# Kernel tuning notes

Hardware: AMD Instinct MI355X
Metric: run time of the kernel (lower is better)

Reference implementation:

```python
import jax, jax.numpy as jnp
import numpy as np

BN_EPS = 1e-5


def setup_inputs() -> dict:
    key = jax.random.key(0)
    ks = jax.random.split(key, 10)
    D, N, NDRUG, NTAIL, NREL = 256, 128, 572, 100000, 100
    return {
        "drug_table": jax.random.normal(ks[0], (NDRUG, D), jnp.float32),
        "rela_table": jax.random.normal(ks[1], (NREL, D), jnp.float32),
        "ent_table": jax.random.normal(ks[2], (NTAIL, D), jnp.float32),
        "W1": jax.random.normal(ks[3], (NDRUG, D, D), jnp.float32),
        "b1": jax.random.normal(ks[4], (N, D), jnp.float32),
        "W2": jax.random.normal(ks[5], (NDRUG, D, D), jnp.float32),
        "b2": jax.random.normal(ks[6], (N, D), jnp.float32),
        "lin_w": jax.random.normal(ks[7], (D, 2 * D), jnp.float32) * (1.0 / np.sqrt(2 * D)),
        "lin_b": jnp.zeros((D,), jnp.float32),
        "bn_gamma": jnp.ones((D,), jnp.float32),
        "bn_beta": jnp.zeros((D,), jnp.float32),
        "drug_name": jnp.arange(NDRUG, dtype=jnp.int64) if jax.config.jax_enable_x64 else jnp.arange(NDRUG, dtype=jnp.int32),
        "adj_tail": jax.random.randint(ks[8], (NDRUG, N), 0, NTAIL, jnp.int32),
        "adj_relation": jax.random.randint(ks[9], (NDRUG, N), 0, NREL, jnp.int32),
    }


def reference(drug_table, rela_table, ent_table, W1, b1, W2, b2,
              lin_w, lin_b, bn_gamma, bn_beta,
              drug_name, adj_tail, adj_relation):
    d = drug_table[drug_name]            # (572, D)
    r = rela_table[adj_relation]         # (572, N, D)
    e = ent_table[adj_tail]              # (572, N, D)

    dr = d[:, None, :] * r               # (572, N, D)
    h = jax.nn.relu(jnp.einsum('bnd,bde->bne', dr, W1) + b1)
    h = jnp.einsum('bnd,bde->bne', h, W2) + b2
    score = jax.nn.softmax(jnp.sum(h, axis=-1), axis=1)   # (572, N)
    w_ent = jnp.einsum('bn,bnd->bd', score, e)             # (572, D)

    x = jnp.concatenate([w_ent, d], axis=1)                # (572, 2D)
    y = jax.nn.relu(x @ lin_w.T + lin_b)                   # (572, D)
    # BatchNorm1d in training mode: batch stats, biased variance
    mean = jnp.mean(y, axis=0)
    var = jnp.var(y, axis=0)
    return bn_gamma * (y - mean) * jax.lax.rsqrt(var + BN_EPS) + bn_beta
```

## Files before the change

kernel.cpp:

```cpp
#include <hip/hip_runtime.h>
#include <math.h>

#define DD   256
#define NN   128
#define NB   572
#define NREL 100
#define KS   32
#define NKS  (DD / KS)
#define EH   128
#define RS   80
#define PSS  132
#define LDRUGS 8

typedef _Float16 h8 __attribute__((ext_vector_type(8)));
typedef _Float16 h2 __attribute__((ext_vector_type(2)));
typedef float    f4 __attribute__((ext_vector_type(4)));

__device__ __forceinline__ float4 ld4(const float* p) {
    return *reinterpret_cast<const float4*>(p);
}
__device__ __forceinline__ void split16(float x, _Float16& hi, _Float16& lo) {
    hi = (_Float16)x;
    lo = (_Float16)(x - (float)hi);
}
__device__ __forceinline__ int slotx(int blk2, int row) {
    return ((blk2 ^ (row & 7)) & 7) * 8;
}

__global__ __launch_bounds__(256)
void sum_rows(const float* __restrict__ W2, const float* __restrict__ b2,
              float* __restrict__ w2s, float* __restrict__ b2s)
{
    const int blk  = blockIdx.x;
    const int tid  = threadIdx.x;
    const int lane = tid & 63;
    const int wv   = tid >> 6;

    if (blk < 2 * NB) {
        const int b = blk >> 1, half = blk & 1;
        const float* src = W2 + (size_t)b * DD * DD + (size_t)half * (DD / 2) * DD;
        float* dst = w2s + (size_t)b * DD + half * (DD / 2);
        for (int r = wv; r < DD / 2; r += 4) {
            float4 v = ld4(&src[r * DD + lane * 4]);
            float s = v.x + v.y + v.z + v.w;
            #pragma unroll
            for (int m = 32; m >= 1; m >>= 1) s += __shfl_xor(s, m, 64);
            if (lane == 0) dst[r] = s;
        }
    } else {
        for (int r = wv; r < NN; r += 4) {
            float4 v = ld4(&b2[r * DD + lane * 4]);
            float s = v.x + v.y + v.z + v.w;
            #pragma unroll
            for (int m = 32; m >= 1; m >>= 1) s += __shfl_xor(s, m, 64);
            if (lane == 0) b2s[r] = s;
        }
    }
}

__global__ __launch_bounds__(512, 4)
void gnn_mm(const float* __restrict__ drug_table,
            const float* __restrict__ rela_table,
            const float* __restrict__ W1,
            const float* __restrict__ b1,
            const int*   __restrict__ drug_name,
            const int*   __restrict__ adj_relation,
            const float* __restrict__ w2s_g,
            float* __restrict__ part)
{
    __shared__ __align__(16) _Float16 AB_l[2 * 128 * RS];
    __shared__ float d_l[DD];
    __shared__ float w2s_l[EH];
    __shared__ int   rel_l[NN], urel_l[NN], head_l[NN], next_l[NN];
    __shared__ int   map_l[NREL];
    __shared__ int   U_l, c0_l;

    _Float16* A_l = AB_l;
    _Float16* B_l = AB_l + 128 * RS;
    float*    Pl  = reinterpret_cast<float*>(AB_l);

    const int bid  = blockIdx.x;
    const int b    = bid >> 1, h = bid & 1;
    const int tid  = threadIdx.x;
    const int lane = tid & 63;
    const int wv   = tid >> 6;
    const int rg   = wv >> 2;
    const int cg   = wv & 3;
    const int r16  = lane & 15;
    const int gb   = lane >> 4;

    if (tid < NN) { rel_l[tid] = adj_relation[b * NN + tid]; head_l[tid] = -1; }
    if (tid < NREL) map_l[tid] = -1;
    if (tid < DD)  d_l[tid] = drug_table[(size_t)drug_name[b] * DD + tid];
    if (tid >= DD && tid < DD + EH)
        w2s_l[tid - DD] = w2s_g[(size_t)b * DD + h * EH + (tid - DD)];
    __syncthreads();
    if (tid < NN) map_l[rel_l[tid]] = 1;
    __syncthreads();

    bool mk = false; int rank = 0, tot = 0;
    if (tid < 128) {
        mk = (tid < NREL) && (map_l[tid] != -1);
        unsigned long long bal = __ballot(mk);
        rank = __popcll(bal & ((1ull << (tid & 63)) - 1));
        tot  = __popcll(bal);
    }
    if (tid < 64) {
        if (mk) { map_l[tid] = rank; urel_l[rank] = tid; }
        if (tid == 0) c0_l = tot;
    }
    __syncthreads();
    if (tid >= 64 && tid < 128) {
        const int base = c0_l;
        if (mk) { map_l[tid] = base + rank; urel_l[base + rank] = tid; }
        if (tid == 64) U_l = base + tot;
    }
    __syncthreads();
    if (tid < NN)
        next_l[tid] = atomicExch(&head_l[map_l[rel_l[tid]]], tid);
    __syncthreads();

    const int U   = U_l;
    const int NRT = (U + 31) >> 5;

    const float* W1b = W1 + (size_t)b * DD * DD;

    {
        const int padrows = NRT * 32 - U;
        h8 z = {(_Float16)0.f,(_Float16)0.f,(_Float16)0.f,(_Float16)0.f,
                (_Float16)0.f,(_Float16)0.f,(_Float16)0.f,(_Float16)0.f};
        for (int x = tid; x < padrows * 8; x += 512) {
            int r = U + (x >> 3), c = (x & 7) * 8;
            *(h8*)&A_l[r * RS + c] = z;
        }
    }

    const int kb  = (tid >> 7) & 3;
    const int be  = tid & 127;
    const int sau = tid >> 2;
    const int sab = tid & 3;

    float rbv[8];
    float4 raA, raB;

    #define STAGE_LOAD(kt_) {                                                  \
        const int k0_ = (kt_) * KS + kb * 8;                                   \
        const float* wp = &W1b[(size_t)k0_ * DD + h * EH + be];                \
        _Pragma("unroll")                                                      \
        for (int j = 0; j < 8; ++j) rbv[j] = wp[(size_t)j * DD];               \
        if (sau < U) {                                                         \
            const float* rr = rela_table + (size_t)urel_l[sau] * DD            \
                              + (kt_) * KS + sab * 8;                          \
            raA = ld4(rr); raB = ld4(rr + 4);                                  \
        }                                                                      \
    }

    #define STAGE_WRITE(kt_) {                                                 \
        const int k0_ = (kt_) * KS + kb * 8;                                   \
        h8 hv, lv;                                                             \
        _Pragma("unroll")                                                      \
        for (int j = 0; j < 8; ++j) {                                          \
            _Float16 hh, ll;                                                   \
            split16(rbv[j] * d_l[k0_ + j], hh, ll);                            \
            hv[j] = hh; lv[j] = ll;                                            \
        }                                                                      \
        *(h8*)&B_l[be * RS + slotx(2 * kb,     be)] = hv;                      \
        *(h8*)&B_l[be * RS + slotx(2 * kb + 1, be)] = lv;                      \
        if (sau < U) {                                                         \
            const float vr[8] = {raA.x, raA.y, raA.z, raA.w,                   \
                                 raB.x, raB.y, raB.z, raB.w};                  \
            h8 ahv, alv;                                                       \
            _Pragma("unroll")                                                  \
            for (int j = 0; j < 8; ++j) {                                      \
                _Float16 hh, ll;                                               \
                split16(vr[j], hh, ll);                                        \
                ahv[j] = hh; alv[j] = ll;                                      \
            }                                                                  \
            *(h8*)&A_l[sau * RS + slotx(2 * sab,     sau)] = ahv;              \
            *(h8*)&A_l[sau * RS + slotx(2 * sab + 1, sau)] = alv;              \
        }                                                                      \
    }

    STAGE_LOAD(0);
    STAGE_WRITE(0);
    __syncthreads();

    f4 acc[2][2][2];
    #pragma unroll
    for (int p = 0; p < 2; ++p)
        #pragma unroll
        for (int sr = 0; sr < 2; ++sr)
            #pragma unroll
            for (int sc = 0; sc < 2; ++sc)
                acc[p][sr][sc] = {0.f, 0.f, 0.f, 0.f};

    for (int kt = 0; kt < NKS; ++kt) {
        if (kt + 1 < NKS) STAGE_LOAD(kt + 1);

        h8 bh[2], bl[2];
        #pragma unroll
        for (int sc = 0; sc < 2; ++sc) {
            const int e = cg * 32 + sc * 16 + r16;
            bh[sc] = *(const h8*)&B_l[e * RS + slotx(2 * gb,     e)];
            bl[sc] = *(const h8*)&B_l[e * RS + slotx(2 * gb + 1, e)];
        }
        #pragma unroll
        for (int p = 0; p < 2; ++p) {
            const int rt = rg + 2 * p;
            if (rt < NRT) {
                #pragma unroll
                for (int sr = 0; sr < 2; ++sr) {
                    const int row = rt * 32 + sr * 16 + r16;
                    h8 ah = *(const h8*)&A_l[row * RS + slotx(2 * gb,     row)];
                    h8 al = *(const h8*)&A_l[row * RS + slotx(2 * gb + 1, row)];
                    #pragma unroll
                    for (int sc = 0; sc < 2; ++sc) {
                        acc[p][sr][sc] = __builtin_amdgcn_mfma_f32_16x16x32_f16(ah, bh[sc], acc[p][sr][sc], 0, 0, 0);
                        acc[p][sr][sc] = __builtin_amdgcn_mfma_f32_16x16x32_f16(al, bh[sc], acc[p][sr][sc], 0, 0, 0);
                        acc[p][sr][sc] = __builtin_amdgcn_mfma_f32_16x16x32_f16(ah, bl[sc], acc[p][sr][sc], 0, 0, 0);
                    }
                }
            }
        }
        __syncthreads();
        if (kt + 1 < NKS) STAGE_WRITE(kt + 1);
        __syncthreads();
    }
    #undef STAGE_LOAD
    #undef STAGE_WRITE

    const int ug   = tid >> 4;
    const int td16 = tid & 15;
    float4 w0 = ld4(&w2s_l[td16 * 8]);
    float4 w1v = ld4(&w2s_l[td16 * 8 + 4]);

    for (int rt = 0; rt < 4; ++rt) {
        if (rt < NRT) {
            __syncthreads();
            if ((rt & 1) == rg) {
                const int p = rt >> 1;
                #pragma unroll
                for (int sr = 0; sr < 2; ++sr)
                    #pragma unroll
                    for (int sc = 0; sc < 2; ++sc)
                        #pragma unroll
                        for (int jj = 0; jj < 4; ++jj)
                            Pl[(sr * 16 + gb * 4 + jj) * PSS + cg * 32 + sc * 16 + r16] =
                                acc[p][sr][sc][jj];
            }
            __syncthreads();
            const int u = rt * 32 + ug;
            if (u < U) {
                float4 p0 = ld4(&Pl[ug * PSS + td16 * 8]);
                float4 p1 = ld4(&Pl[ug * PSS + td16 * 8 + 4]);
                int n = head_l[u];
                while (n >= 0) {
                    const float* bp = b1 + (size_t)n * DD + h * EH + td16 * 8;
                    float4 b0 = ld4(bp);
                    float4 b1v = ld4(bp + 4);
                    float s = fmaxf(p0.x + b0.x,  0.f) * w0.x
                            + fmaxf(p0.y + b0.y,  0.f) * w0.y
                            + fmaxf(p0.z + b0.z,  0.f) * w0.z
                            + fmaxf(p0.w + b0.w,  0.f) * w0.w
                            + fmaxf(p1.x + b1v.x, 0.f) * w1v.x
                            + fmaxf(p1.y + b1v.y, 0.f) * w1v.y
                            + fmaxf(p1.z + b1v.z, 0.f) * w1v.z
                            + fmaxf(p1.w + b1v.w, 0.f) * w1v.w;
                    #pragma unroll
                    for (int m = 8; m >= 1; m >>= 1) s += __shfl_xor(s, m, 16);
                    if (td16 == 0) part[(size_t)b * 256 + h * NN + n] = s;
                    n = next_l[n];
                }
            }
        }
    }
}

__global__ __launch_bounds__(256)
void gnn_gather(const float* __restrict__ drug_table,
                const float* __restrict__ ent_table,
                const int*   __restrict__ drug_name,
                const int*   __restrict__ adj_tail,
                const float* __restrict__ part,
                const float* __restrict__ b2s_g,
                float* __restrict__ xbuf)
{
    __shared__ float score_l[NN];
    __shared__ int   tail_l[NN];

    const int b = blockIdx.x, tid = threadIdx.x;

    if (tid < NN) {
        tail_l[tid]  = adj_tail[b * NN + tid];
        score_l[tid] = part[(size_t)b * 256 + tid]
                     + part[(size_t)b * 256 + NN + tid] + b2s_g[tid];
    }
    __syncthreads();

    if (tid < 64) {
        float l0 = score_l[tid], l1 = score_l[tid + 64];
        float M = fmaxf(l0, l1);
        #pragma unroll
        for (int m = 32; m >= 1; m >>= 1) M = fmaxf(M, __shfl_xor(M, m, 64));
        float e0 = expf(l0 - M), e1 = expf(l1 - M);
        float S = e0 + e1;
        #pragma unroll
        for (int m = 32; m >= 1; m >>= 1) S += __shfl_xor(S, m, 64);
        float inv = 1.f / S;
        score_l[tid]      = e0 * inv;
        score_l[tid + 64] = e1 * inv;
    }
    __syncthreads();

    float w = 0.f;
    for (int n = 0; n < NN; ++n) {
        float s = score_l[n];
        if (s > 1e-9f)
            w = fmaf(s, ent_table[(size_t)tail_l[n] * DD + tid], w);
    }
    xbuf[(size_t)b * 512 + tid]       = w;
    xbuf[(size_t)b * 512 + 256 + tid] = drug_table[(size_t)drug_name[b] * DD + tid];
}

__global__ __launch_bounds__(256)
void gnn_lin(const float* __restrict__ lin_w,
             const float* __restrict__ lin_b,
             const float* __restrict__ xbuf,
             float* __restrict__ Y)
{
    __shared__ float x_l[LDRUGS * 512];

    const int g = blockIdx.x, tid = threadIdx.x;
    const int b0 = g * LDRUGS;

    #pragma unroll
    for (int i = 0; i < LDRUGS * 2; ++i) {
        int f = tid + i * 256;
        *reinterpret_cast<float4*>(&x_l[f * 4]) = ld4(&xbuf[(size_t)b0 * 512 + f * 4]);
    }
    __syncthreads();

    const float* lw = lin_w + (size_t)tid * 512;
    float dot[LDRUGS];
    #pragma unroll
    for (int d = 0; d < LDRUGS; ++d) dot[d] = 0.f;

    for (int k4 = 0; k4 < 128; ++k4) {
        float4 wv = ld4(&lw[k4 * 4]);
        #pragma unroll
        for (int d = 0; d < LDRUGS; ++d) {
            float4 xv = ld4(&x_l[d * 512 + k4 * 4]);
            dot[d] += wv.x * xv.x + wv.y * xv.y + wv.z * xv.z + wv.w * xv.w;
        }
    }

    const float bb = lin_b[tid];
    #pragma unroll
    for (int d = 0; d < LDRUGS; ++d) {
        if (b0 + d < NB)
            Y[(size_t)(b0 + d) * DD + tid] = fmaxf(dot[d] + bb, 0.f);
    }
}

__global__ void bn_stats(const float* __restrict__ Y, float* __restrict__ stats)
{
    int d = blockIdx.x, t = threadIdx.x;
    float s = 0.f, ss = 0.f;
    for (int b = t; b < NB; b += 64) {
        float v = Y[(size_t)b * DD + d];
        s += v; ss += v * v;
    }
    #pragma unroll
    for (int m = 32; m >= 1; m >>= 1) {
        s  += __shfl_xor(s, m, 64);
        ss += __shfl_xor(ss, m, 64);
    }
    if (t == 0) {
        float mean = s * (1.f / NB);
        float var  = ss * (1.f / NB) - mean * mean;
        stats[d]      = mean;
        stats[DD + d] = rsqrtf(var + 1e-5f);
    }
}

__global__ void bn_apply(float* __restrict__ Y, const float* __restrict__ stats,
                         const float* __restrict__ gamma, const float* __restrict__ beta)
{
    int b = blockIdx.x, t = threadIdx.x;
    float mean = stats[t], inv = stats[DD + t];
    float v = Y[(size_t)b * DD + t];
    Y[(size_t)b * DD + t] = gamma[t] * (v - mean) * inv + beta[t];
}

extern "C" void kernel_launch(void* const* d_in, const int* in_sizes, int n_in,
                              void* d_out, int out_size, void* d_ws, size_t ws_size,
                              hipStream_t stream)
{
    const float* drug_table = (const float*)d_in[0];
    const float* rela_table = (const float*)d_in[1];
    const float* ent_table  = (const float*)d_in[2];
    const float* W1         = (const float*)d_in[3];
    const float* b1         = (const float*)d_in[4];
    const float* W2         = (const float*)d_in[5];
    const float* b2         = (const float*)d_in[6];
    const float* lin_w      = (const float*)d_in[7];
    const float* lin_b      = (const float*)d_in[8];
    const float* bn_g       = (const float*)d_in[9];
    const float* bn_b       = (const float*)d_in[10];
    const int*   drug_name  = (const int*)d_in[11];
    const int*   adj_tail   = (const int*)d_in[12];
    const int*   adj_rel    = (const int*)d_in[13];
    float* out = (float*)d_out;

    const int NBP = ((NB + LDRUGS - 1) / LDRUGS) * LDRUGS;
    float* w2s   = (float*)d_ws;
    float* b2s   = w2s + (size_t)NB * DD;
    float* part  = b2s + NN;
    float* xbuf  = part + (size_t)NB * 256;
    float* stats = xbuf + (size_t)NBP * 512;

    sum_rows<<<2 * NB + 1, 256, 0, stream>>>(W2, b2, w2s, b2s);
    gnn_mm<<<2 * NB, 512, 0, stream>>>(drug_table, rela_table, W1, b1,
                                       drug_name, adj_rel, w2s, part);
    gnn_gather<<<NB, 256, 0, stream>>>(drug_table, ent_table, drug_name,
                                       adj_tail, part, b2s, xbuf);
    gnn_lin<<<NBP / LDRUGS, 256, 0, stream>>>(lin_w, lin_b, xbuf, out);
    bn_stats<<<DD, 64, 0, stream>>>(out, stats);
    bn_apply<<<NB, DD, 0, stream>>>(out, stats, bn_g, bn_b);
}
```

Before: 132.5 us.

## Split gnn_mm output columns into four quarters with 256-thread blocks

Changes the GEMM kernel's work split from two 128-column halves per drug with 512 threads to four 64-column quarters per drug with 256 threads, so the grid grows to 4*NB blocks. LDS use per block shrinks, which could let more blocks fit per CU and balances work across more CUs. The cost is that each block re-stages the full relation A tile (now loaded by half as many threads) and repeats the dedup setup four times per drug, and the gather kernel must sum four partial score arrays instead of two.

```diff
diff --git a/kernel.cpp b/kernel.cpp
--- a/kernel.cpp
+++ b/kernel.cpp
@@ -7,13 +7,12 @@
 #define NREL 100
 #define KS   32
 #define NKS  (DD / KS)
-#define EH   128
+#define EQ   64
 #define RS   80
-#define PSS  132
+#define PSS  68
 #define LDRUGS 8
 
 typedef _Float16 h8 __attribute__((ext_vector_type(8)));
-typedef _Float16 h2 __attribute__((ext_vector_type(2)));
 typedef float    f4 __attribute__((ext_vector_type(4)));
 
 __device__ __forceinline__ float4 ld4(const float* p) {
@@ -58,7 +57,7 @@
     }
 }
 
-__global__ __launch_bounds__(512, 4)
+__global__ __launch_bounds__(256, 4)
 void gnn_mm(const float* __restrict__ drug_table,
             const float* __restrict__ rela_table,
             const float* __restrict__ W1,
@@ -68,9 +67,9 @@
             const float* __restrict__ w2s_g,
             float* __restrict__ part)
 {
-    __shared__ __align__(16) _Float16 AB_l[2 * 128 * RS];
+    __shared__ __align__(16) _Float16 AB_l[(128 + EQ) * RS];
     __shared__ float d_l[DD];
-    __shared__ float w2s_l[EH];
+    __shared__ float w2s_l[EQ];
     __shared__ int   rel_l[NN], urel_l[NN], head_l[NN], next_l[NN];
     __shared__ int   map_l[NREL];
     __shared__ int   U_l, c0_l;
@@ -80,20 +79,19 @@
     float*    Pl  = reinterpret_cast<float*>(AB_l);
 
     const int bid  = blockIdx.x;
-    const int b    = bid >> 1, h = bid & 1;
+    const int b    = bid >> 2, q = bid & 3;
     const int tid  = threadIdx.x;
     const int lane = tid & 63;
     const int wv   = tid >> 6;
-    const int rg   = wv >> 2;
-    const int cg   = wv & 3;
+    const int rg   = wv >> 1;
+    const int cg   = wv & 1;
     const int r16  = lane & 15;
     const int gb   = lane >> 4;
 
     if (tid < NN) { rel_l[tid] = adj_relation[b * NN + tid]; head_l[tid] = -1; }
     if (tid < NREL) map_l[tid] = -1;
-    if (tid < DD)  d_l[tid] = drug_table[(size_t)drug_name[b] * DD + tid];
-    if (tid >= DD && tid < DD + EH)
-        w2s_l[tid - DD] = w2s_g[(size_t)b * DD + h * EH + (tid - DD)];
+    d_l[tid] = drug_table[(size_t)drug_name[b] * DD + tid];
+    if (tid >= 192) w2s_l[tid - 192] = w2s_g[(size_t)b * DD + q * EQ + (tid - 192)];
     __syncthreads();
     if (tid < NN) map_l[rel_l[tid]] = 1;
     __syncthreads();
@@ -129,29 +127,30 @@
         const int padrows = NRT * 32 - U;
         h8 z = {(_Float16)0.f,(_Float16)0.f,(_Float16)0.f,(_Float16)0.f,
                 (_Float16)0.f,(_Float16)0.f,(_Float16)0.f,(_Float16)0.f};
-        for (int x = tid; x < padrows * 8; x += 512) {
+        for (int x = tid; x < padrows * 8; x += 256) {
             int r = U + (x >> 3), c = (x & 7) * 8;
             *(h8*)&A_l[r * RS + c] = z;
         }
     }
 
-    const int kb  = (tid >> 7) & 3;
-    const int be  = tid & 127;
-    const int sau = tid >> 2;
-    const int sab = tid & 3;
+    const int kb  = tid >> 6;
+    const int be  = tid & 63;
+    const int sau = tid >> 1;
+    const int sa2 = (tid & 1) * 2;
 
     float rbv[8];
-    float4 raA, raB;
+    float4 raA, raB, raC, raD;
 
     #define STAGE_LOAD(kt_) {                                                  \
         const int k0_ = (kt_) * KS + kb * 8;                                   \
-        const float* wp = &W1b[(size_t)k0_ * DD + h * EH + be];                \
+        const float* wp = &W1b[(size_t)k0_ * DD + q * EQ + be];                \
         _Pragma("unroll")                                                      \
         for (int j = 0; j < 8; ++j) rbv[j] = wp[(size_t)j * DD];               \
         if (sau < U) {                                                         \
             const float* rr = rela_table + (size_t)urel_l[sau] * DD            \
-                              + (kt_) * KS + sab * 8;                          \
-            raA = ld4(rr); raB = ld4(rr + 4);                                  \
+                              + (kt_) * KS + sa2 * 8;                          \
+            raA = ld4(rr);     raB = ld4(rr + 4);                              \
+            raC = ld4(rr + 8); raD = ld4(rr + 12);                             \
         }                                                                      \
     }
 
@@ -167,17 +166,23 @@
         *(h8*)&B_l[be * RS + slotx(2 * kb,     be)] = hv;                      \
         *(h8*)&B_l[be * RS + slotx(2 * kb + 1, be)] = lv;                      \
         if (sau < U) {                                                         \
-            const float vr[8] = {raA.x, raA.y, raA.z, raA.w,                   \
-                                 raB.x, raB.y, raB.z, raB.w};                  \
-            h8 ahv, alv;                                                       \
+            const float vr[16] = {raA.x, raA.y, raA.z, raA.w,                  \
+                                  raB.x, raB.y, raB.z, raB.w,                  \
+                                  raC.x, raC.y, raC.z, raC.w,                  \
+                                  raD.x, raD.y, raD.z, raD.w};                 \
             _Pragma("unroll")                                                  \
-            for (int j = 0; j < 8; ++j) {                                      \
-                _Float16 hh, ll;                                               \
-                split16(vr[j], hh, ll);                                        \
-                ahv[j] = hh; alv[j] = ll;                                      \
+            for (int o = 0; o < 2; ++o) {                                      \
+                const int oct = sa2 + o;                                       \
+                h8 ahv, alv;                                                   \
+                _Pragma("unroll")                                              \
+                for (int j = 0; j < 8; ++j) {                                  \
+                    _Float16 hh, ll;                                           \
+                    split16(vr[o * 8 + j], hh, ll);                            \
+                    ahv[j] = hh; alv[j] = ll;                                  \
+                }                                                              \
+                *(h8*)&A_l[sau * RS + slotx(2 * oct,     sau)] = ahv;          \
+                *(h8*)&A_l[sau * RS + slotx(2 * oct + 1, sau)] = alv;          \
             }                                                                  \
-            *(h8*)&A_l[sau * RS + slotx(2 * sab,     sau)] = ahv;              \
-            *(h8*)&A_l[sau * RS + slotx(2 * sab + 1, sau)] = alv;              \
         }                                                                      \
     }
 
@@ -229,10 +234,10 @@
     #undef STAGE_LOAD
     #undef STAGE_WRITE
 
-    const int ug   = tid >> 4;
-    const int td16 = tid & 15;
-    float4 w0 = ld4(&w2s_l[td16 * 8]);
-    float4 w1v = ld4(&w2s_l[td16 * 8 + 4]);
+    const int ug  = tid >> 3;
+    const int td8 = tid & 7;
+    float4 w0  = ld4(&w2s_l[td8 * 8]);
+    float4 w1v = ld4(&w2s_l[td8 * 8 + 4]);
 
     for (int rt = 0; rt < 4; ++rt) {
         if (rt < NRT) {
@@ -251,11 +256,11 @@
             __syncthreads();
             const int u = rt * 32 + ug;
             if (u < U) {
-                float4 p0 = ld4(&Pl[ug * PSS + td16 * 8]);
-                float4 p1 = ld4(&Pl[ug * PSS + td16 * 8 + 4]);
+                float4 p0 = ld4(&Pl[ug * PSS + td8 * 8]);
+                float4 p1 = ld4(&Pl[ug * PSS + td8 * 8 + 4]);
                 int n = head_l[u];
                 while (n >= 0) {
-                    const float* bp = b1 + (size_t)n * DD + h * EH + td16 * 8;
+                    const float* bp = b1 + (size_t)n * DD + q * EQ + td8 * 8;
                     float4 b0 = ld4(bp);
                     float4 b1v = ld4(bp + 4);
                     float s = fmaxf(p0.x + b0.x,  0.f) * w0.x
@@ -267,8 +272,8 @@
                             + fmaxf(p1.z + b1v.z, 0.f) * w1v.z
                             + fmaxf(p1.w + b1v.w, 0.f) * w1v.w;
                     #pragma unroll
-                    for (int m = 8; m >= 1; m >>= 1) s += __shfl_xor(s, m, 16);
-                    if (td16 == 0) part[(size_t)b * 256 + h * NN + n] = s;
+                    for (int m = 4; m >= 1; m >>= 1) s += __shfl_xor(s, m, 8);
+                    if (td8 == 0) part[(size_t)(b * 4 + q) * NN + n] = s;
                     n = next_l[n];
                 }
             }
@@ -292,8 +297,8 @@
 
     if (tid < NN) {
         tail_l[tid]  = adj_tail[b * NN + tid];
-        score_l[tid] = part[(size_t)b * 256 + tid]
-                     + part[(size_t)b * 256 + NN + tid] + b2s_g[tid];
+        const float* pp = part + (size_t)b * 4 * NN + tid;
+        score_l[tid] = pp[0] + pp[NN] + pp[2 * NN] + pp[3 * NN] + b2s_g[tid];
     }
     __syncthreads();
 
@@ -416,11 +421,11 @@
     float* w2s   = (float*)d_ws;
     float* b2s   = w2s + (size_t)NB * DD;
     float* part  = b2s + NN;
-    float* xbuf  = part + (size_t)NB * 256;
+    float* xbuf  = part + (size_t)NB * 4 * NN;
     float* stats = xbuf + (size_t)NBP * 512;
 
     sum_rows<<<2 * NB + 1, 256, 0, stream>>>(W2, b2, w2s, b2s);
-    gnn_mm<<<2 * NB, 512, 0, stream>>>(drug_table, rela_table, W1, b1,
+    gnn_mm<<<4 * NB, 256, 0, stream>>>(drug_table, rela_table, W1, b1,
                                        drug_name, adj_rel, w2s, part);
     gnn_gather<<<NB, 256, 0, stream>>>(drug_table, ent_table, drug_name,
                                        adj_tail, part, b2s, xbuf);
```

Result: no change. 135.0 us (+1.9%).
